# Optimization experiments

Hardware: AMD Instinct MI355X
Metric: run time of the kernel (lower is better)

Reference implementation:

```python
import jax, jax.numpy as jnp
import numpy as np

MARGIN = 2.0
EPS = 1e-6  # F.pairwise_distance default: norm of (x1 - x2 + eps)

N, D = 4096, 768


def setup_inputs() -> dict:
    key = jax.random.key(0)
    k1, k2, k3 = jax.random.split(key, 3)
    image_embedding = jax.random.normal(k1, (N, D), dtype=jnp.float32)
    text_embedding = jax.random.normal(k2, (N, D), dtype=jnp.float32)
    ground_truth = jax.random.randint(k3, (N, N), 0, 2, dtype=jnp.int32)
    return {
        "image_embedding": image_embedding,
        "text_embedding": text_embedding,
        "ground_truth": ground_truth,
    }


def reference(image_embedding, text_embedding, ground_truth):
    d = image_embedding.shape[1]
    # Pairwise squared distance with pairwise_distance's +eps on the diff:
    # ||a - b + eps||^2 = ||a||^2 + ||b||^2 - 2 a.b + 2 eps (sum a - sum b) + d eps^2
    sa = jnp.sum(image_embedding * image_embedding, axis=1)   # [n]
    sb = jnp.sum(text_embedding * text_embedding, axis=1)     # [n]
    dot = image_embedding @ text_embedding.T                  # [n, n]
    ra = jnp.sum(image_embedding, axis=1)                     # [n]
    rb = jnp.sum(text_embedding, axis=1)                      # [n]
    sq = (sa[:, None] + sb[None, :] - 2.0 * dot
          + 2.0 * EPS * (ra[:, None] - rb[None, :]) + d * EPS * EPS)
    dist = jnp.sqrt(jnp.maximum(sq, 0.0))                     # [n, n]
    label = ground_truth.astype(dist.dtype)
    hinge = jnp.maximum(MARGIN - dist, 0.0)
    loss = jnp.mean((1.0 - label) * dist * dist + label * hinge * hinge)
    return loss
```

## Files before the change

kernel.cpp:

```cpp
#include <hip/hip_runtime.h>
#include <hip/hip_bf16.h>
#include <stdint.h>
#include <stddef.h>


#define NROWS 4096
#define DIM   768
#define BM    128
#define BN    128
#define BKE   128
#define KITERS (DIM / BKE)
#define MARGIN 2.0f
#define EPSV   1e-6f

typedef float f32x4 __attribute__((ext_vector_type(4)));
typedef unsigned long long u64;
typedef unsigned char fp8_t;

__global__ __launch_bounds__(256) void prologue_kernel(
    const float* __restrict__ A, const float* __restrict__ B,
    const int* __restrict__ gt,
    fp8_t* __restrict__ Af8, fp8_t* __restrict__ Bf8,
    float* __restrict__ sa, float* __restrict__ sb,
    float* __restrict__ ra, float* __restrict__ rb,
    u64* __restrict__ gtp, float* __restrict__ out)
{
    const int tid  = threadIdx.x;
    const int wave = tid >> 6;
    const int lane = tid & 63;
    const int bx   = blockIdx.x;

    if (bx == 0 && tid == 0) out[0] = 0.0f;

    if (bx < 2048) {
        const int isB  = bx >= 1024;
        const int row  = (bx & 1023) * 4 + wave;
        const float* X = isB ? B : A;
        fp8_t* Xb      = isB ? Bf8 : Af8;
        float* sdst    = isB ? sb : sa;
        float* rdst    = isB ? rb : ra;

        const float4* xr = (const float4*)(X + (size_t)row * DIM);
        unsigned int* xb = (unsigned int*)(Xb + (size_t)row * DIM);

        float sum = 0.0f, sq = 0.0f;
        #pragma unroll
        for (int j = 0; j < 3; ++j) {
            float4 v = xr[lane + 64 * j];
            int pk = 0;
            pk = __builtin_amdgcn_cvt_pk_fp8_f32(v.x, v.y, pk, false);
            pk = __builtin_amdgcn_cvt_pk_fp8_f32(v.z, v.w, pk, true);
            xb[lane + 64 * j] = (unsigned int)pk;
            sum += (v.x + v.y) + (v.z + v.w);
            sq  += v.x * v.x + v.y * v.y + v.z * v.z + v.w * v.w;
        }
        #pragma unroll
        for (int off = 32; off > 0; off >>= 1) {
            sum += __shfl_down(sum, off);
            sq  += __shfl_down(sq,  off);
        }
        if (lane == 0) { rdst[row] = sum; sdst[row] = sq; }
    } else {
        const int wid = (bx - 2048) * 4 + wave;
        const size_t base = (size_t)wid * 8;
        int v[8];
        #pragma unroll
        for (int i = 0; i < 8; ++i)
            v[i] = gt[base * 64 + (size_t)i * 64 + lane];
        u64 mine = 0;
        #pragma unroll
        for (int i = 0; i < 8; ++i) {
            const u64 m = __ballot(v[i] != 0);
            if (lane == i) mine = m;
        }
        if (lane < 8) gtp[base + lane] = mine;
    }
}

__global__ __launch_bounds__(256, 4) void loss_kernel(
    const fp8_t* __restrict__ A, const fp8_t* __restrict__ B,
    const float* __restrict__ sa, const float* __restrict__ sb,
    const float* __restrict__ ra, const float* __restrict__ rb,
    const uint2* __restrict__ gtp, float* __restrict__ out)
{
    __shared__ __align__(16) fp8_t As[BM * BKE];
    __shared__ __align__(16) fp8_t Bs[BN * BKE];

    const int tid  = threadIdx.x;
    const int wave = tid >> 6;
    const int lane = tid & 63;
    const int m0 = blockIdx.y * BM;
    const int n0 = blockIdx.x * BN;

    f32x4 acc[4][4] = {};

    const int fr = lane & 15;
    const int q  = lane >> 4;
    const int wm = (wave >> 1) * 64;
    const int wn = (wave & 1) * 64;

    const int srow = lane >> 3;
    const int sp   = lane & 7;

    for (int k0 = 0; k0 < DIM; k0 += BKE) {
        __syncthreads();
        #pragma unroll
        for (int j = 0; j < 4; ++j) {
            const int c0  = wave * 256 + j * 64;
            const int row = (c0 >> 3) + srow;
            const int gcx = sp ^ (row & 7);
            const fp8_t* ga = A + (size_t)(m0 + row) * DIM + k0 + gcx * 16;
            __builtin_amdgcn_global_load_lds(
                (const __attribute__((address_space(1))) void*)ga,
                (__attribute__((address_space(3))) void*)(As + c0 * 16),
                16, 0, 0);
        }
        #pragma unroll
        for (int j = 0; j < 4; ++j) {
            const int c0  = wave * 256 + j * 64;
            const int row = (c0 >> 3) + srow;
            const int gcx = sp ^ (row & 7);
            const fp8_t* gb = B + (size_t)(n0 + row) * DIM + k0 + gcx * 16;
            __builtin_amdgcn_global_load_lds(
                (const __attribute__((address_space(1))) void*)gb,
                (__attribute__((address_space(3))) void*)(Bs + c0 * 16),
                16, 0, 0);
        }
        __syncthreads();

        #pragma unroll
        for (int kk = 0; kk < 4; ++kk) {
            const int c = kk * 2 + (q >> 1);
            const int h = (q & 1) * 8;
            long af[4], bfr[4];
            #pragma unroll
            for (int i = 0; i < 4; ++i) {
                const int ra_ = wm + i * 16 + fr;
                const int rb_ = wn + i * 16 + fr;
                af[i]  = *(const long*)(As + ra_ * BKE + (c ^ (ra_ & 7)) * 16 + h);
                bfr[i] = *(const long*)(Bs + rb_ * BKE + (c ^ (rb_ & 7)) * 16 + h);
            }
            #pragma unroll
            for (int mi = 0; mi < 4; ++mi)
                #pragma unroll
                for (int ni = 0; ni < 4; ++ni)
                    acc[mi][ni] = __builtin_amdgcn_mfma_f32_16x16x32_fp8_fp8(
                        af[mi], bfr[ni], acc[mi][ni], 0, 0, 0);
        }
    }

    const int cq = lane & 15;
    const int rq = (lane >> 4) * 4;
    const int cb = (n0 + wn) >> 6;

    float cc[4];
    #pragma unroll
    for (int ni = 0; ni < 4; ++ni) {
        const int col = n0 + wn + ni * 16 + cq;
        cc[ni] = sb[col] - 2.0f * EPSV * rb[col];
    }

    float s_all = 0.0f, s_g = 0.0f, dmin = 1e30f;
    #pragma unroll
    for (int mi = 0; mi < 4; ++mi) {
        #pragma unroll
        for (int rr = 0; rr < 4; ++rr) {
            const int row = m0 + wm + mi * 16 + rq + rr;
            const float crr = sa[row] + 2.0f * EPSV * ra[row]
                            + (float)DIM * EPSV * EPSV;
            const uint2 w = gtp[(size_t)row * (NROWS / 64) + cb];
            #pragma unroll
            for (int ni = 0; ni < 4; ++ni) {
                const float d2 = (crr + cc[ni]) - 2.0f * acc[mi][ni][rr];
                s_all += d2;
                dmin = fminf(dmin, d2);
                const unsigned wd = (ni < 2) ? w.x : w.y;
                const float gf = (float)((wd >> (cq + (ni & 1) * 16)) & 1u);
                s_g = fmaf(gf, d2, s_g);
            }
        }
    }
    float local = s_all - s_g;

    if (dmin < 4.0f) {
        #pragma unroll
        for (int mi = 0; mi < 4; ++mi) {
            #pragma unroll
            for (int rr = 0; rr < 4; ++rr) {
                const int row = m0 + wm + mi * 16 + rq + rr;
                const float crr = sa[row] + 2.0f * EPSV * ra[row]
                                + (float)DIM * EPSV * EPSV;
                const uint2 w = gtp[(size_t)row * (NROWS / 64) + cb];
                #pragma unroll
                for (int ni = 0; ni < 4; ++ni) {
                    const float d2 = (crr + cc[ni]) - 2.0f * acc[mi][ni][rr];
                    if (d2 < 4.0f) {
                        const unsigned wd = (ni < 2) ? w.x : w.y;
                        const float gf = (float)((wd >> (cq + (ni & 1) * 16)) & 1u);
                        const float d2c  = fmaxf(d2, 0.0f);
                        const float dist = sqrtf(d2c);
                        const float h    = fmaxf(MARGIN - dist, 0.0f);
                        local += (1.0f - gf) * d2c + gf * h * h - (d2 - gf * d2);
                    }
                }
            }
        }
    }

    #pragma unroll
    for (int off = 32; off > 0; off >>= 1) local += __shfl_down(local, off);

    float* redp = (float*)As;
    __syncthreads();
    if (lane == 0) redp[wave] = local;
    __syncthreads();
    if (tid == 0) {
        const float s = (redp[0] + redp[1]) + (redp[2] + redp[3]);
        atomicAdd(out, s * (1.0f / (4096.0f * 4096.0f)));
    }
}

extern "C" void kernel_launch(void* const* d_in, const int* in_sizes, int n_in,
                              void* d_out, int out_size, void* d_ws, size_t ws_size,
                              hipStream_t stream)
{
    const float* A  = (const float*)d_in[0];
    const float* B  = (const float*)d_in[1];
    const int*   gt = (const int*)d_in[2];
    float* out = (float*)d_out;

    char* ws = (char*)d_ws;
    const size_t NB8 = (size_t)NROWS * DIM;
    fp8_t* Af8 = (fp8_t*)(ws);
    fp8_t* Bf8 = (fp8_t*)(ws + NB8);
    float* sa = (float*)(ws + 2 * NB8);
    float* sb = (float*)(ws + 2 * NB8 + 16384);
    float* ra = (float*)(ws + 2 * NB8 + 32768);
    float* rb = (float*)(ws + 2 * NB8 + 49152);
    u64* gtp  = (u64*)(ws + 2 * NB8 + 65536);

    prologue_kernel<<<dim3(10240), 256, 0, stream>>>(
        A, B, gt, Af8, Bf8, sa, sb, ra, rb, gtp, out);
    loss_kernel<<<dim3(NROWS / BN, NROWS / BM), 256, 0, stream>>>(
        Af8, Bf8, sa, sb, ra, rb, (const uint2*)gtp, out);
}
```

Baseline: 155.6 us.

## Pre-permute fp8 K layout to load 16-byte LDS fragments and merge epilogue passes

The prologue writes the fp8 copies with a permuted K ordering inside each 128-byte segment. Each lane can then read one 16-byte vector from LDS that feeds two consecutive MFMA k-steps, replacing two 8-byte reads and halving LDS read instructions. The epilogue is also folded into a single pass with a rarely-taken branch for the d2<4 hinge case, dropping the second recomputation loop. Correctness relies on A and B both being permuted the same way so the dot products are unchanged.

Result: faster. 136.0 us (median of 2 runs) (-12.6%).

```diff
diff --git a/kernel.cpp b/kernel.cpp
--- a/kernel.cpp
+++ b/kernel.cpp
@@ -9,13 +9,14 @@
 #define BM    128
 #define BN    128
 #define BKE   128
-#define KITERS (DIM / BKE)
 #define MARGIN 2.0f
 #define EPSV   1e-6f
 
 typedef float f32x4 __attribute__((ext_vector_type(4)));
+typedef long  lng2  __attribute__((ext_vector_type(2)));
 typedef unsigned long long u64;
 typedef unsigned char fp8_t;
+
 
 __global__ __launch_bounds__(256) void prologue_kernel(
     const float* __restrict__ A, const float* __restrict__ B,
@@ -45,12 +46,19 @@
 
         float sum = 0.0f, sq = 0.0f;
         #pragma unroll
-        for (int j = 0; j < 3; ++j) {
-            float4 v = xr[lane + 64 * j];
+        for (int jb = 0; jb < 3; ++jb) {
+            float4 v = xr[lane + 64 * jb];
             int pk = 0;
             pk = __builtin_amdgcn_cvt_pk_fp8_f32(v.x, v.y, pk, false);
             pk = __builtin_amdgcn_cvt_pk_fp8_f32(v.z, v.w, pk, true);
-            xb[lane + 64 * j] = (unsigned int)pk;
+            const int e4  = lane + 64 * jb;
+            const int seg = e4 >> 5;
+            const int e   = (e4 & 31) * 4;
+            const int kk  = e >> 5;
+            const int q   = (e >> 3) & 3;
+            const int jj  = e & 7;
+            const int pos = ((kk >> 1) * 4 + q) * 16 + (kk & 1) * 8 + jj;
+            xb[seg * 32 + (pos >> 2)] = (unsigned int)pk;
             sum += (v.x + v.y) + (v.z + v.w);
             sq  += v.x * v.x + v.y * v.y + v.z * v.z + v.w * v.w;
         }
@@ -129,23 +137,28 @@
         __syncthreads();
 
         #pragma unroll
-        for (int kk = 0; kk < 4; ++kk) {
-            const int c = kk * 2 + (q >> 1);
-            const int h = (q & 1) * 8;
-            long af[4], bfr[4];
+        for (int kk2 = 0; kk2 < 2; ++kk2) {
+            const int c = kk2 * 4 + q;
+            lng2 ap[4], bp[4];
             #pragma unroll
             for (int i = 0; i < 4; ++i) {
-                const int ra_ = wm + i * 16 + fr;
-                const int rb_ = wn + i * 16 + fr;
-                af[i]  = *(const long*)(As + ra_ * BKE + (c ^ (ra_ & 7)) * 16 + h);
-                bfr[i] = *(const long*)(Bs + rb_ * BKE + (c ^ (rb_ & 7)) * 16 + h);
+                const int ar = wm + i * 16 + fr;
+                const int br = wn + i * 16 + fr;
+                ap[i] = *(const lng2*)(As + ar * BKE + ((c ^ (ar & 7)) * 16));
+                bp[i] = *(const lng2*)(Bs + br * BKE + ((c ^ (br & 7)) * 16));
             }
             #pragma unroll
             for (int mi = 0; mi < 4; ++mi)
                 #pragma unroll
                 for (int ni = 0; ni < 4; ++ni)
                     acc[mi][ni] = __builtin_amdgcn_mfma_f32_16x16x32_fp8_fp8(
-                        af[mi], bfr[ni], acc[mi][ni], 0, 0, 0);
+                        ap[mi][0], bp[ni][0], acc[mi][ni], 0, 0, 0);
+            #pragma unroll
+            for (int mi = 0; mi < 4; ++mi)
+                #pragma unroll
+                for (int ni = 0; ni < 4; ++ni)
+                    acc[mi][ni] = __builtin_amdgcn_mfma_f32_16x16x32_fp8_fp8(
+                        ap[mi][1], bp[ni][1], acc[mi][ni], 0, 0, 0);
         }
     }
 
@@ -160,7 +173,7 @@
         cc[ni] = sb[col] - 2.0f * EPSV * rb[col];
     }
 
-    float s_all = 0.0f, s_g = 0.0f, dmin = 1e30f;
+    float local = 0.0f;
     #pragma unroll
     for (int mi = 0; mi < 4; ++mi) {
         #pragma unroll
@@ -172,37 +185,16 @@
             #pragma unroll
             for (int ni = 0; ni < 4; ++ni) {
                 const float d2 = (crr + cc[ni]) - 2.0f * acc[mi][ni][rr];
-                s_all += d2;
-                dmin = fminf(dmin, d2);
                 const unsigned wd = (ni < 2) ? w.x : w.y;
                 const float gf = (float)((wd >> (cq + (ni & 1) * 16)) & 1u);
-                s_g = fmaf(gf, d2, s_g);
-            }
-        }
-    }
-    float local = s_all - s_g;
-
-    if (dmin < 4.0f) {
-        #pragma unroll
-        for (int mi = 0; mi < 4; ++mi) {
-            #pragma unroll
-            for (int rr = 0; rr < 4; ++rr) {
-                const int row = m0 + wm + mi * 16 + rq + rr;
-                const float crr = sa[row] + 2.0f * EPSV * ra[row]
-                                + (float)DIM * EPSV * EPSV;
-                const uint2 w = gtp[(size_t)row * (NROWS / 64) + cb];
-                #pragma unroll
-                for (int ni = 0; ni < 4; ++ni) {
-                    const float d2 = (crr + cc[ni]) - 2.0f * acc[mi][ni][rr];
-                    if (d2 < 4.0f) {
-                        const unsigned wd = (ni < 2) ? w.x : w.y;
-                        const float gf = (float)((wd >> (cq + (ni & 1) * 16)) & 1u);
-                        const float d2c  = fmaxf(d2, 0.0f);
-                        const float dist = sqrtf(d2c);
-                        const float h    = fmaxf(MARGIN - dist, 0.0f);
-                        local += (1.0f - gf) * d2c + gf * h * h - (d2 - gf * d2);
-                    }
+                float contrib = d2 - gf * d2;
+                if (__builtin_expect(d2 < 4.0f, 0)) {
+                    const float d2c  = fmaxf(d2, 0.0f);
+                    const float dist = sqrtf(d2c);
+                    const float h    = fmaxf(MARGIN - dist, 0.0f);
+                    contrib = (1.0f - gf) * d2c + gf * h * h;
                 }
+                local += contrib;
             }
         }
     }
```
